# Kernel optimization log

Hardware: AMD Instinct MI355X
Metric: run time of the kernel (lower is better)

Reference implementation:

```python
import jax, jax.numpy as jnp
import numpy as np

HEADS = 8
DQK = 64
DV = 64
SPAN = 32
STRIDE = 1


def setup_inputs() -> dict:
    key = jax.random.key(0)
    ks = jax.random.split(key, 7)
    B, Lq, Lkv = 2, 4096, 4096
    dq = dk = dv = 512
    dout = 512
    w_scale = 0.02
    return {
        "q": jax.random.normal(ks[0], (B, Lq, dq), jnp.float32),
        "k": jax.random.normal(ks[1], (B, Lkv, dk), jnp.float32),
        "v": jax.random.normal(ks[2], (B, Lkv, dv), jnp.float32),
        "Wq": jax.random.normal(ks[3], (dq, HEADS * DQK), jnp.float32) * w_scale,
        "Wk": jax.random.normal(ks[4], (dk, HEADS * DQK), jnp.float32) * w_scale,
        "Wv": jax.random.normal(ks[5], (dv, HEADS * DV), jnp.float32) * w_scale,
        "Wo": jax.random.normal(ks[6], (HEADS * DV, dout), jnp.float32) * w_scale,
    }


def reference(q, k, v, Wq, Wk, Wv, Wo):
    B, Lq, _ = q.shape
    Lkv = k.shape[1]
    # projections -> [B, H, L, d]
    Q = (q @ Wq).reshape(B, Lq, HEADS, DQK).transpose(0, 2, 1, 3)
    K = (k @ Wk).reshape(B, Lkv, HEADS, DQK).transpose(0, 2, 1, 3)
    V = (v @ Wv).reshape(B, Lkv, HEADS, DV).transpose(0, 2, 1, 3)

    # sliding window indices: kvi[r, j] = r - (span-1) + stride*j  -> [span, Lq]
    r = jnp.arange(SPAN)
    j = jnp.arange(Lq)
    kvi = r[:, None] - (SPAN - 1) + STRIDE * j[None, :]
    valid = (kvi >= 0) & (kvi < Lkv)                      # [span, Lq]
    kvs = jnp.clip(kvi, 0, Lkv - 1)

    Kg = K[:, :, kvs, :]                                   # [B, H, span, Lq, dQK]
    scores = jnp.einsum("bhjd,bhrjd->bhrj", Q, Kg) / (DQK ** 0.5)
    scores = jnp.where(valid, scores, -jnp.inf)
    # faithful to original: softmax over dim=3 == length_q axis
    W = jax.nn.softmax(scores, axis=3)                     # [B, H, span, Lq]
    W = jnp.where(valid, W, 0.0)

    Vg = V[:, :, kvs, :]                                   # [B, H, span, Lq, dV]
    O = jnp.einsum("bhrj,bhrjd->bhjd", W, Vg)              # sum over span
    out = O.transpose(0, 2, 1, 3).reshape(B, Lq, HEADS * DV) @ Wo
    return out
```

## Files before the change

kernel.cpp:

```cpp
#include <hip/hip_runtime.h>
#include <hip/hip_bf16.h>

#define L_Q 4096
#define NB 2
#define DMODEL 512
#define NHEAD 8
#define DHEAD 64
#define SPAN_ 32

using short8 = __attribute__((ext_vector_type(8))) short;
using f32x4  = __attribute__((ext_vector_type(4))) float;

typedef __attribute__((address_space(1))) const void GV;
typedef __attribute__((address_space(3))) void LV;

__device__ __forceinline__ void gl2lds16(const void* g, void* l) {
    __builtin_amdgcn_global_load_lds((GV*)g, (LV*)l, 16, 0, 0);
}

__device__ __forceinline__ float bf2f(short u) {
    return __uint_as_float(((unsigned)(unsigned short)u) << 16);
}
__device__ __forceinline__ short f2bf(float f) {
    __hip_bfloat16 h = __float2bfloat16(f);
    return *reinterpret_cast<short*>(&h);
}
__device__ __forceinline__ unsigned packbf(float lo, float hi) {
    return (unsigned)(unsigned short)f2bf(lo) | ((unsigned)(unsigned short)f2bf(hi) << 16);
}

__global__ __launch_bounds__(256) void castT4_bf16(
    const float* __restrict__ Wq, const float* __restrict__ Wk,
    const float* __restrict__ Wv, const float* __restrict__ Wo,
    short* __restrict__ Wtq, short* __restrict__ Wtk,
    short* __restrict__ Wtv, short* __restrict__ Wto)
{
    const int z = blockIdx.z;
    const float* W = (z == 0) ? Wq : ((z == 1) ? Wk : ((z == 2) ? Wv : Wo));
    short* Wt = (z == 0) ? Wtq : ((z == 1) ? Wtk : ((z == 2) ? Wtv : Wto));
    __shared__ float t[32][33];
    const int tx = threadIdx.x, ty = threadIdx.y;
    const int bx = blockIdx.x, by = blockIdx.y;
#pragma unroll
    for (int i = 0; i < 4; ++i)
        t[ty + i * 8][tx] = W[(size_t)(by * 32 + ty + i * 8) * DMODEL + bx * 32 + tx];
    __syncthreads();
#pragma unroll
    for (int i = 0; i < 4; ++i)
        Wt[(size_t)(bx * 32 + ty + i * 8) * DMODEL + by * 32 + tx] = f2bf(t[tx][ty + i * 8]);
}

template<int OUTMODE, bool ACAST>
__device__ __forceinline__ void gemm128_body(
    const void* __restrict__ Avoid, const short* __restrict__ Bt, void* __restrict__ Cout,
    short* As, short* Bs)
{
    const int tid = threadIdx.x;
    const int m0 = blockIdx.y * 128;
    const int n0 = blockIdx.x * 128;
    const int w = tid >> 6, lane = tid & 63;
    const int wr = w & 1, wc = w >> 1;
    const int l15 = lane & 15, l4 = lane >> 4;

    f32x4 acc[4][4];
#pragma unroll
    for (int fm = 0; fm < 4; ++fm)
#pragma unroll
        for (int fn = 0; fn < 4; ++fn) acc[fm][fn] = (f32x4){0.f, 0.f, 0.f, 0.f};

    for (int k0 = 0; k0 < DMODEL; k0 += 64) {
        __syncthreads();
        if (ACAST) {
            const float* Af = (const float*)Avoid;
#pragma unroll
            for (int it = 0; it < 4; ++it) {
                int c = it * 256 + tid;
                int row = c >> 3, slot = c & 7;
                const float* src = Af + (size_t)(m0 + row) * DMODEL + k0 + slot * 8;
                float4 a = *(const float4*)src;
                float4 b = *(const float4*)(src + 4);
                short8 o;
                o[0] = f2bf(a.x); o[1] = f2bf(a.y); o[2] = f2bf(a.z); o[3] = f2bf(a.w);
                o[4] = f2bf(b.x); o[5] = f2bf(b.y); o[6] = f2bf(b.z); o[7] = f2bf(b.w);
                *(short8*)&As[(row * 8 + (slot ^ (row & 7))) * 8] = o;
            }
        } else {
            const short* Ab = (const short*)Avoid;
#pragma unroll
            for (int it = 0; it < 4; ++it) {
                int c = it * 256 + tid;
                int row = c >> 3, slot = c & 7;
                gl2lds16(Ab + (size_t)(m0 + row) * DMODEL + k0 + ((slot ^ (row & 7)) << 3), &As[c * 8]);
            }
        }
#pragma unroll
        for (int it = 0; it < 4; ++it) {
            int c = it * 256 + tid;
            int row = c >> 3, slot = c & 7;
            gl2lds16(Bt + (size_t)(n0 + row) * DMODEL + k0 + ((slot ^ (row & 7)) << 3), &Bs[c * 8]);
        }
        __syncthreads();
#pragma unroll
        for (int ks = 0; ks < 2; ++ks) {
            const int koff = ks * 4 + l4;
            short8 a[4], b[4];
#pragma unroll
            for (int fm = 0; fm < 4; ++fm) {
                int row = wr * 64 + fm * 16 + l15;
                a[fm] = *(const short8*)&As[(row * 8 + (koff ^ (row & 7))) * 8];
            }
#pragma unroll
            for (int fn = 0; fn < 4; ++fn) {
                int row = wc * 64 + fn * 16 + l15;
                b[fn] = *(const short8*)&Bs[(row * 8 + (koff ^ (row & 7))) * 8];
            }
#pragma unroll
            for (int fm = 0; fm < 4; ++fm)
#pragma unroll
                for (int fn = 0; fn < 4; ++fn)
                    acc[fm][fn] = __builtin_amdgcn_mfma_f32_16x16x32_bf16(
                        a[fm], b[fn], acc[fm][fn], 0, 0, 0);
        }
    }
#pragma unroll
    for (int fm = 0; fm < 4; ++fm)
#pragma unroll
        for (int fn = 0; fn < 4; ++fn) {
            if (OUTMODE == 2) {
                short4 o4;
                o4.x = f2bf(acc[fm][fn][0]);
                o4.y = f2bf(acc[fm][fn][1]);
                o4.z = f2bf(acc[fm][fn][2]);
                o4.w = f2bf(acc[fm][fn][3]);
                int m = m0 + wr * 64 + fm * 16 + l4 * 4;
                int bb = m >> 12, g = m & (L_Q - 1);
                int n = n0 + wc * 64 + fn * 16 + l15;
                int hh = n >> 6, dd = n & 63;
                *(short4*)&((short*)Cout)[(((size_t)bb * NHEAD + hh) * DHEAD + dd) * L_Q + g] = o4;
            } else {
#pragma unroll
                for (int i = 0; i < 4; ++i) {
                    size_t row = (size_t)(m0 + wr * 64 + fm * 16 + l4 * 4 + i);
                    int col = n0 + wc * 64 + fn * 16 + l15;
                    if (OUTMODE == 1) ((short*)Cout)[row * DMODEL + col] = f2bf(acc[fm][fn][i]);
                    else              ((float*)Cout)[row * DMODEL + col] = acc[fm][fn][i];
                }
            }
        }
}

__global__ __launch_bounds__(256) void gemm_qkv(
    const float* __restrict__ q, const float* __restrict__ k, const float* __restrict__ v,
    const short* __restrict__ Wtq, const short* __restrict__ Wtk, const short* __restrict__ Wtv,
    short* __restrict__ Qp, short* __restrict__ Kp, short* __restrict__ Vt)
{
    __shared__ short As[128 * 64];
    __shared__ short Bs[128 * 64];
    const int z = blockIdx.z;
    const float* A  = (z == 0) ? q   : ((z == 1) ? k   : v);
    const short* Bt = (z == 0) ? Wtq : ((z == 1) ? Wtk : Wtv);
    if (z == 2) gemm128_body<2, true>(A, Bt, Vt, As, Bs);
    else        gemm128_body<1, true>(A, Bt, (z == 0) ? Qp : Kp, As, Bs);
}

__global__ __launch_bounds__(256) void gemm_fin(
    const short* __restrict__ Op, const short* __restrict__ Wto, float* __restrict__ out)
{
    __shared__ short As[128 * 64];
    __shared__ short Bs[128 * 64];
    gemm128_body<0, false>(Op, Wto, out, As, Bs);
}

__global__ __launch_bounds__(256) void attn_e(
    const short* __restrict__ Qp, const short* __restrict__ Kp,
    float* __restrict__ part)
{
    __shared__ short Ks[160 * 64];
    __shared__ short Qs[128 * 64];
    __shared__ float eb[128][36];
    __shared__ float red[8][32];
    const int tid = threadIdx.x;
    const int j0 = blockIdx.x * 128;
    const int h = blockIdx.y, b = blockIdx.z;
    const int bh = b * NHEAD + h;
    const int w = tid >> 6, lane = tid & 63;
    const int l15 = lane & 15, l4 = lane >> 4;

    {
        float4 z = make_float4(0.f, 0.f, 0.f, 0.f);
        float4* ebv = (float4*)&eb[0][0];
#pragma unroll
        for (int i = 0; i < 5; ++i) {
            int idx = i * 256 + tid;
            if (idx < 1152) ebv[idx] = z;
        }
    }
#pragma unroll
    for (int it = 0; it < 5; ++it) {
        int c = it * 256 + tid;
        int row = c >> 3, slot = c & 7;
        int g = j0 - 31 + row;
        g = (g < 0) ? 0 : ((g > L_Q - 1) ? L_Q - 1 : g);
        gl2lds16(Kp + ((size_t)b * L_Q + g) * DMODEL + h * DHEAD + ((slot ^ (row & 7)) << 3), &Ks[c * 8]);
    }
#pragma unroll
    for (int it = 0; it < 4; ++it) {
        int c = it * 256 + tid;
        int row = c >> 3, slot = c & 7;
        gl2lds16(Qp + ((size_t)b * L_Q + j0 + row) * DMODEL + h * DHEAD + ((slot ^ (row & 7)) << 3), &Qs[c * 8]);
    }
    __syncthreads();

    f32x4 acc[2][4];
#pragma unroll
    for (int tm = 0; tm < 2; ++tm)
#pragma unroll
        for (int tn = 0; tn < 4; ++tn) acc[tm][tn] = (f32x4){0.f, 0.f, 0.f, 0.f};
#pragma unroll
    for (int kk = 0; kk < 2; ++kk) {
        const int koff = kk * 4 + l4;
        short8 af[2], bf[4];
#pragma unroll
        for (int tm = 0; tm < 2; ++tm) {
            int row = w * 32 + tm * 16 + l15;
            af[tm] = *(const short8*)&Qs[(row * 8 + (koff ^ (row & 7))) * 8];
        }
#pragma unroll
        for (int tn = 0; tn < 4; ++tn) {
            int row = w * 32 + tn * 16 + l15;
            bf[tn] = *(const short8*)&Ks[(row * 8 + (koff ^ (row & 7))) * 8];
        }
#pragma unroll
        for (int tm = 0; tm < 2; ++tm)
#pragma unroll
            for (int tn = 0; tn < 4; ++tn)
                acc[tm][tn] = __builtin_amdgcn_mfma_f32_16x16x32_bf16(
                    af[tm], bf[tn], acc[tm][tn], 0, 0, 0);
    }

    const int gbase = j0 + w * 32 - 31;
#pragma unroll
    for (int tm = 0; tm < 2; ++tm)
#pragma unroll
        for (int tn = 0; tn < 4; ++tn)
#pragma unroll
            for (int i = 0; i < 4; ++i) {
                int q = tm * 16 + l4 * 4 + i;
                int rr = tn * 16 + l15;
                int r = rr - q;
                bool valid = (r >= 0) && (r < SPAN_) && (gbase + rr >= 0);
                if (valid) eb[w * 32 + q][r] = __expf(acc[tm][tn][i] * 0.125f);
            }
    __syncthreads();

    {
        int r = tid & 31, grp = tid >> 5;
        float s = 0.f;
#pragma unroll
        for (int qq = 0; qq < 16; ++qq) s += eb[grp * 16 + qq][r];
        red[grp][r] = s;
    }
    __syncthreads();
    if (tid < 32) {
        float s = 0.f;
#pragma unroll
        for (int g = 0; g < 8; ++g) s += red[g][tid];
        part[((size_t)bh * SPAN_ + tid) * 32 + blockIdx.x] = s;
    }
}

__global__ __launch_bounds__(256) void attn_o(
    const short* __restrict__ Qp, const short* __restrict__ Kp,
    const short* __restrict__ Vt, const float* __restrict__ part,
    short* __restrict__ Op)
{
    __shared__ short Ks[160 * 64];
    __shared__ short Qs[128 * 64];
    __shared__ short Vts[64 * 192];
    const int tid = threadIdx.x;
    const int j0 = blockIdx.x * 128;
    const int h = blockIdx.y, b = blockIdx.z;
    const int bh = b * NHEAD + h;
    const int w = tid >> 6, lane = tid & 63;
    const int l15 = lane & 15, l4 = lane >> 4;

#pragma unroll
    for (int it = 0; it < 5; ++it) {
        int c = it * 256 + tid;
        int row = c >> 3, slot = c & 7;
        int g = j0 - 32 + row;
        g = (g < 0) ? 0 : ((g > L_Q - 1) ? L_Q - 1 : g);
        gl2lds16(Kp + ((size_t)b * L_Q + g) * DMODEL + h * DHEAD + ((slot ^ (row & 7)) << 3), &Ks[c * 8]);
    }
#pragma unroll
    for (int it = 0; it < 4; ++it) {
        int c = it * 256 + tid;
        int row = c >> 3, slot = c & 7;
        gl2lds16(Qp + ((size_t)b * L_Q + j0 + row) * DMODEL + h * DHEAD + ((slot ^ (row & 7)) << 3), &Qs[c * 8]);
    }
#pragma unroll
    for (int it = 0; it < 6; ++it) {
        int c = it * 256 + tid;
        int d = c / 24, cs = c - d * 24;
        int gg = j0 - 32 + ((cs ^ (d & 7)) << 3);
        gg = (gg < 0) ? 0 : ((gg > L_Q - 8) ? L_Q - 8 : gg);
        gl2lds16(Vt + ((size_t)bh * DHEAD + d) * L_Q + gg, &Vts[c * 8]);
    }

    float iv;
    {
        const float4* pp = (const float4*)(part + ((size_t)bh * SPAN_ + (lane & 31)) * 32);
        float s = 0.f;
#pragma unroll
        for (int i = 0; i < 8; ++i) {
            float4 t = pp[i];
            s += t.x + t.y + t.z + t.w;
        }
        iv = 1.0f / s;
    }
    __syncthreads();

    f32x4 sa[4][2];
#pragma unroll
    for (int tk = 0; tk < 4; ++tk)
#pragma unroll
        for (int tq = 0; tq < 2; ++tq) sa[tk][tq] = (f32x4){0.f, 0.f, 0.f, 0.f};
#pragma unroll
    for (int kk = 0; kk < 2; ++kk) {
        const int koff = kk * 4 + l4;
        short8 af[4], qf[2];
#pragma unroll
        for (int tk = 0; tk < 4; ++tk) {
            int row = w * 32 + tk * 16 + l15;
            af[tk] = *(const short8*)&Ks[(row * 8 + (koff ^ (row & 7))) * 8];
        }
#pragma unroll
        for (int tq = 0; tq < 2; ++tq) {
            int row = w * 32 + tq * 16 + l15;
            qf[tq] = *(const short8*)&Qs[(row * 8 + (koff ^ (row & 7))) * 8];
        }
#pragma unroll
        for (int tk = 0; tk < 4; ++tk)
#pragma unroll
            for (int tq = 0; tq < 2; ++tq)
                sa[tk][tq] = __builtin_amdgcn_mfma_f32_16x16x32_bf16(
                    af[tk], qf[tq], sa[tk][tq], 0, 0, 0);
    }

    const int gbase = j0 + w * 32 - 32;
#pragma unroll
    for (int tk = 0; tk < 4; ++tk)
#pragma unroll
        for (int tq = 0; tq < 2; ++tq)
#pragma unroll
            for (int i = 0; i < 4; ++i) {
                int rrp = tk * 16 + l4 * 4 + i;
                int q = tq * 16 + l15;
                int r = rrp - q - 1;
                bool valid = (r >= 0) && (r < SPAN_) && (gbase + rrp >= 0);
                float e = __expf(sa[tk][tq][i] * 0.125f) * __shfl(iv, r & 31);
                sa[tk][tq][i] = valid ? e : 0.f;
            }

    unsigned pk[4][2][2];
#pragma unroll
    for (int tk = 0; tk < 4; ++tk)
#pragma unroll
        for (int tq = 0; tq < 2; ++tq) {
            pk[tk][tq][0] = packbf(sa[tk][tq][0], sa[tk][tq][1]);
            pk[tk][tq][1] = packbf(sa[tk][tq][2], sa[tk][tq][3]);
        }

    const int hi = l4 >> 1;
    const int lsA = ((l4 & 1) << 5) + l15;

    f32x4 oa[2][4];
#pragma unroll
    for (int tm = 0; tm < 2; ++tm)
#pragma unroll
        for (int dn = 0; dn < 4; ++dn) oa[tm][dn] = (f32x4){0.f, 0.f, 0.f, 0.f};
#pragma unroll
    for (int kk = 0; kk < 2; ++kk) {
        short8 pa[2];
#pragma unroll
        for (int tm = 0; tm < 2; ++tm) {
            unsigned lo00 = (unsigned)__shfl((int)pk[kk * 2 + 0][tm][0], lsA);
            unsigned hi00 = (unsigned)__shfl((int)pk[kk * 2 + 1][tm][0], lsA);
            unsigned lo01 = (unsigned)__shfl((int)pk[kk * 2 + 0][tm][1], lsA);
            unsigned hi01 = (unsigned)__shfl((int)pk[kk * 2 + 1][tm][1], lsA);
            unsigned lo10 = (unsigned)__shfl((int)pk[kk * 2 + 0][tm][0], lsA + 16);
            unsigned hi10 = (unsigned)__shfl((int)pk[kk * 2 + 1][tm][0], lsA + 16);
            unsigned lo11 = (unsigned)__shfl((int)pk[kk * 2 + 0][tm][1], lsA + 16);
            unsigned hi11 = (unsigned)__shfl((int)pk[kk * 2 + 1][tm][1], lsA + 16);
            uint4 wds;
            wds.x = hi ? hi00 : lo00;
            wds.y = hi ? hi01 : lo01;
            wds.z = hi ? hi10 : lo10;
            wds.w = hi ? hi11 : lo11;
            pa[tm] = *reinterpret_cast<short8*>(&wds);
        }
#pragma unroll
        for (int dn = 0; dn < 4; ++dn) {
            int row = dn * 16 + l15;
            int cs = w * 4 + kk * 4 + l4;
            short8 vb = *(const short8*)&Vts[row * 192 + ((cs ^ (row & 7)) << 3)];
#pragma unroll
            for (int tm = 0; tm < 2; ++tm)
                oa[tm][dn] = __builtin_amdgcn_mfma_f32_16x16x32_bf16(
                    pa[tm], vb, oa[tm][dn], 0, 0, 0);
        }
    }

#pragma unroll
    for (int tm = 0; tm < 2; ++tm)
#pragma unroll
        for (int dn = 0; dn < 4; ++dn)
#pragma unroll
            for (int i = 0; i < 4; ++i) {
                int q = w * 32 + tm * 16 + l4 * 4 + i;
                Op[((size_t)b * L_Q + j0 + q) * DMODEL + h * DHEAD + dn * 16 + l15] =
                    f2bf(oa[tm][dn][i]);
            }
}

extern "C" void kernel_launch(void* const* d_in, const int* in_sizes, int n_in,
                              void* d_out, int out_size, void* d_ws, size_t ws_size,
                              hipStream_t stream) {
    (void)in_sizes; (void)n_in; (void)out_size; (void)ws_size;
    const float* q  = (const float*)d_in[0];
    const float* k  = (const float*)d_in[1];
    const float* v  = (const float*)d_in[2];
    const float* Wq = (const float*)d_in[3];
    const float* Wk = (const float*)d_in[4];
    const float* Wv = (const float*)d_in[5];
    const float* Wo = (const float*)d_in[6];
    float* out = (float*)d_out;

    char* ws = (char*)d_ws;
    const size_t MiB = 1ull << 20;
    short* Wtq = (short*)(ws);
    short* Wtk = (short*)(ws + 512 * 1024);
    short* Wtv = (short*)(ws + 1 * MiB);
    short* Wto = (short*)(ws + 1 * MiB + 512 * 1024);
    short* Qp  = (short*)(ws + 2 * MiB);
    short* Kp  = (short*)(ws + 10 * MiB);
    short* Vtp = (short*)(ws + 18 * MiB);
    short* Op  = (short*)(ws + 26 * MiB);
    float* part = (float*)(ws + 34 * MiB);

    castT4_bf16<<<dim3(16, 16, 4), dim3(32, 8), 0, stream>>>(
        Wq, Wk, Wv, Wo, Wtq, Wtk, Wtv, Wto);

    gemm_qkv<<<dim3(4, 64, 3), 256, 0, stream>>>(q, k, v, Wtq, Wtk, Wtv, Qp, Kp, Vtp);

    dim3 ga(L_Q / 128, NHEAD, NB);
    attn_e<<<ga, 256, 0, stream>>>(Qp, Kp, part);
    attn_o<<<ga, 256, 0, stream>>>(Qp, Kp, Vtp, part, Op);

    gemm_fin<<<dim3(4, 64), 256, 0, stream>>>(Op, Wto, out);
}
```

Baseline: 77.31 us.

## Prefetch fp32 A tiles into registers and swizzle GEMM blocks across XCDs

The GEMM body now loads the next k-slice of the fp32 A operand into registers while MFMAs on the current slice run, so global load latency for the cast path overlaps compute. Block indices are also remapped so that consecutive hardware block IDs (round-robined over the 8 XCDs) place the tiles of one M-row group on the same XCD, improving L2 reuse of A and B. This costs 32 extra VGPRs for the prefetch buffer, which may reduce occupancy. The swizzle hardcodes a 4x64 tile grid.

```diff
diff --git a/kernel.cpp b/kernel.cpp
--- a/kernel.cpp
+++ b/kernel.cpp
@@ -50,35 +50,52 @@
         Wt[(size_t)(bx * 32 + ty + i * 8) * DMODEL + by * 32 + tx] = f2bf(t[tx][ty + i * 8]);
 }
 
+__device__ __forceinline__ void xcd_swizzle(int& m0, int& n0) {
+    int hw = blockIdx.x + (blockIdx.y << 2);
+    int xcd = hw & 7, slot = hw >> 3;
+    int mt = xcd * 8 + (slot >> 2);
+    int nt = slot & 3;
+    m0 = mt * 128;
+    n0 = nt * 128;
+}
+
 template<int OUTMODE, bool ACAST>
 __device__ __forceinline__ void gemm128_body(
     const void* __restrict__ Avoid, const short* __restrict__ Bt, void* __restrict__ Cout,
-    short* As, short* Bs)
+    short* As, short* Bs, int m0, int n0)
 {
     const int tid = threadIdx.x;
-    const int m0 = blockIdx.y * 128;
-    const int n0 = blockIdx.x * 128;
     const int w = tid >> 6, lane = tid & 63;
     const int wr = w & 1, wc = w >> 1;
     const int l15 = lane & 15, l4 = lane >> 4;
+    const float* Af = (const float*)Avoid;
 
     f32x4 acc[4][4];
 #pragma unroll
     for (int fm = 0; fm < 4; ++fm)
 #pragma unroll
         for (int fn = 0; fn < 4; ++fn) acc[fm][fn] = (f32x4){0.f, 0.f, 0.f, 0.f};
+
+    float4 pf[8];
+    if (ACAST) {
+#pragma unroll
+        for (int it = 0; it < 4; ++it) {
+            int c = it * 256 + tid;
+            int row = c >> 3, slot = c & 7;
+            const float* src = Af + (size_t)(m0 + row) * DMODEL + slot * 8;
+            pf[it * 2 + 0] = *(const float4*)src;
+            pf[it * 2 + 1] = *(const float4*)(src + 4);
+        }
+    }
 
     for (int k0 = 0; k0 < DMODEL; k0 += 64) {
         __syncthreads();
         if (ACAST) {
-            const float* Af = (const float*)Avoid;
 #pragma unroll
             for (int it = 0; it < 4; ++it) {
                 int c = it * 256 + tid;
                 int row = c >> 3, slot = c & 7;
-                const float* src = Af + (size_t)(m0 + row) * DMODEL + k0 + slot * 8;
-                float4 a = *(const float4*)src;
-                float4 b = *(const float4*)(src + 4);
+                float4 a = pf[it * 2 + 0], b = pf[it * 2 + 1];
                 short8 o;
                 o[0] = f2bf(a.x); o[1] = f2bf(a.y); o[2] = f2bf(a.z); o[3] = f2bf(a.w);
                 o[4] = f2bf(b.x); o[5] = f2bf(b.y); o[6] = f2bf(b.z); o[7] = f2bf(b.w);
@@ -100,6 +117,16 @@
             gl2lds16(Bt + (size_t)(n0 + row) * DMODEL + k0 + ((slot ^ (row & 7)) << 3), &Bs[c * 8]);
         }
         __syncthreads();
+        if (ACAST && k0 + 64 < DMODEL) {
+#pragma unroll
+            for (int it = 0; it < 4; ++it) {
+                int c = it * 256 + tid;
+                int row = c >> 3, slot = c & 7;
+                const float* src = Af + (size_t)(m0 + row) * DMODEL + (k0 + 64) + slot * 8;
+                pf[it * 2 + 0] = *(const float4*)src;
+                pf[it * 2 + 1] = *(const float4*)(src + 4);
+            }
+        }
 #pragma unroll
         for (int ks = 0; ks < 2; ++ks) {
             const int koff = ks * 4 + l4;
@@ -156,11 +183,13 @@
 {
     __shared__ short As[128 * 64];
     __shared__ short Bs[128 * 64];
+    int m0, n0;
+    xcd_swizzle(m0, n0);
     const int z = blockIdx.z;
     const float* A  = (z == 0) ? q   : ((z == 1) ? k   : v);
     const short* Bt = (z == 0) ? Wtq : ((z == 1) ? Wtk : Wtv);
-    if (z == 2) gemm128_body<2, true>(A, Bt, Vt, As, Bs);
-    else        gemm128_body<1, true>(A, Bt, (z == 0) ? Qp : Kp, As, Bs);
+    if (z == 2) gemm128_body<2, true>(A, Bt, Vt, As, Bs, m0, n0);
+    else        gemm128_body<1, true>(A, Bt, (z == 0) ? Qp : Kp, As, Bs, m0, n0);
 }
 
 __global__ __launch_bounds__(256) void gemm_fin(
@@ -168,7 +197,9 @@
 {
     __shared__ short As[128 * 64];
     __shared__ short Bs[128 * 64];
-    gemm128_body<0, false>(Op, Wto, out, As, Bs);
+    int m0, n0;
+    xcd_swizzle(m0, n0);
+    gemm128_body<0, false>(Op, Wto, out, As, Bs, m0, n0);
 }
 
 __global__ __launch_bounds__(256) void attn_e(
```

Measured after the change: 63.25 us (median of 2 runs). 18.2% less time.

## Load fp32 A tiles via direct-to-LDS and swizzle GEMM blocks across XCDs

Applied to the files above, without the earlier changes.

The QKV projection GEMM now streams fp32 activations straight into LDS with async global_load_lds and converts them to bf16 when it reads fragments, instead of loading into registers, converting, and storing to LDS. Both GEMMs also remap block indices so that consecutive M tiles sharing the same rows land on the same XCD, which is meant to improve L2 reuse. In exchange, the fp32 A tile doubles LDS use to 32KB and the conversion now runs redundantly inside the MFMA inner loop. The swizzle hardcodes a grid of 4 N tiles by 64 M tiles.

```diff
diff --git a/kernel.cpp b/kernel.cpp
--- a/kernel.cpp
+++ b/kernel.cpp
@@ -50,17 +50,26 @@
         Wt[(size_t)(bx * 32 + ty + i * 8) * DMODEL + by * 32 + tx] = f2bf(t[tx][ty + i * 8]);
 }
 
-template<int OUTMODE, bool ACAST>
+__device__ __forceinline__ void xcd_swizzle(int& m0, int& n0) {
+    int hw = blockIdx.x + (blockIdx.y << 2);
+    int xcd = hw & 7, slot = hw >> 3;
+    int mt = xcd * 8 + (slot >> 2);
+    int nt = slot & 3;
+    m0 = mt * 128;
+    n0 = nt * 128;
+}
+
+template<int OUTMODE, bool AF32>
 __device__ __forceinline__ void gemm128_body(
     const void* __restrict__ Avoid, const short* __restrict__ Bt, void* __restrict__ Cout,
-    short* As, short* Bs)
+    void* AsRaw, short* Bs, int m0, int n0)
 {
     const int tid = threadIdx.x;
-    const int m0 = blockIdx.y * 128;
-    const int n0 = blockIdx.x * 128;
     const int w = tid >> 6, lane = tid & 63;
     const int wr = w & 1, wc = w >> 1;
     const int l15 = lane & 15, l4 = lane >> 4;
+    float* Asf = (float*)AsRaw;
+    short* Asb = (short*)AsRaw;
 
     f32x4 acc[4][4];
 #pragma unroll
@@ -70,27 +79,23 @@
 
     for (int k0 = 0; k0 < DMODEL; k0 += 64) {
         __syncthreads();
-        if (ACAST) {
+        if (AF32) {
             const float* Af = (const float*)Avoid;
+#pragma unroll
+            for (int it = 0; it < 8; ++it) {
+                int c = it * 256 + tid;
+                int row = c >> 4, slot = c & 15;
+                gl2lds16(Af + (size_t)(m0 + row) * DMODEL + k0 + ((slot ^ (row & 15)) << 2),
+                         &Asf[c * 4]);
+            }
+        } else {
+            const short* Ab = (const short*)Avoid;
 #pragma unroll
             for (int it = 0; it < 4; ++it) {
                 int c = it * 256 + tid;
                 int row = c >> 3, slot = c & 7;
-                const float* src = Af + (size_t)(m0 + row) * DMODEL + k0 + slot * 8;
-                float4 a = *(const float4*)src;
-                float4 b = *(const float4*)(src + 4);
-                short8 o;
-                o[0] = f2bf(a.x); o[1] = f2bf(a.y); o[2] = f2bf(a.z); o[3] = f2bf(a.w);
-                o[4] = f2bf(b.x); o[5] = f2bf(b.y); o[6] = f2bf(b.z); o[7] = f2bf(b.w);
-                *(short8*)&As[(row * 8 + (slot ^ (row & 7))) * 8] = o;
-            }
-        } else {
-            const short* Ab = (const short*)Avoid;
-#pragma unroll
-            for (int it = 0; it < 4; ++it) {
-                int c = it * 256 + tid;
-                int row = c >> 3, slot = c & 7;
-                gl2lds16(Ab + (size_t)(m0 + row) * DMODEL + k0 + ((slot ^ (row & 7)) << 3), &As[c * 8]);
+                gl2lds16(Ab + (size_t)(m0 + row) * DMODEL + k0 + ((slot ^ (row & 7)) << 3),
+                         &Asb[c * 8]);
             }
         }
 #pragma unroll
@@ -107,7 +112,17 @@
 #pragma unroll
             for (int fm = 0; fm < 4; ++fm) {
                 int row = wr * 64 + fm * 16 + l15;
-                a[fm] = *(const short8*)&As[(row * 8 + (koff ^ (row & 7))) * 8];
+                if (AF32) {
+                    int rx = row & 15;
+                    float4 f0 = *(const float4*)&Asf[row * 64 + (((koff * 2)     ^ rx) << 2)];
+                    float4 f1 = *(const float4*)&Asf[row * 64 + (((koff * 2 + 1) ^ rx) << 2)];
+                    short8 o;
+                    o[0] = f2bf(f0.x); o[1] = f2bf(f0.y); o[2] = f2bf(f0.z); o[3] = f2bf(f0.w);
+                    o[4] = f2bf(f1.x); o[5] = f2bf(f1.y); o[6] = f2bf(f1.z); o[7] = f2bf(f1.w);
+                    a[fm] = o;
+                } else {
+                    a[fm] = *(const short8*)&Asb[(row * 8 + (koff ^ (row & 7))) * 8];
+                }
             }
 #pragma unroll
             for (int fn = 0; fn < 4; ++fn) {
@@ -154,13 +169,15 @@
     const short* __restrict__ Wtq, const short* __restrict__ Wtk, const short* __restrict__ Wtv,
     short* __restrict__ Qp, short* __restrict__ Kp, short* __restrict__ Vt)
 {
-    __shared__ short As[128 * 64];
+    __shared__ float Asf[128 * 64];
     __shared__ short Bs[128 * 64];
+    int m0, n0;
+    xcd_swizzle(m0, n0);
     const int z = blockIdx.z;
     const float* A  = (z == 0) ? q   : ((z == 1) ? k   : v);
     const short* Bt = (z == 0) ? Wtq : ((z == 1) ? Wtk : Wtv);
-    if (z == 2) gemm128_body<2, true>(A, Bt, Vt, As, Bs);
-    else        gemm128_body<1, true>(A, Bt, (z == 0) ? Qp : Kp, As, Bs);
+    if (z == 2) gemm128_body<2, true>(A, Bt, Vt, Asf, Bs, m0, n0);
+    else        gemm128_body<1, true>(A, Bt, (z == 0) ? Qp : Kp, Asf, Bs, m0, n0);
 }
 
 __global__ __launch_bounds__(256) void gemm_fin(
@@ -168,7 +185,9 @@
 {
     __shared__ short As[128 * 64];
     __shared__ short Bs[128 * 64];
-    gemm128_body<0, false>(Op, Wto, out, As, Bs);
+    int m0, n0;
+    xcd_swizzle(m0, n0);
+    gemm128_body<0, false>(Op, Wto, out, As, Bs, m0, n0);
 }
 
 __global__ __launch_bounds__(256) void attn_e(
```

Measured after the change: 64.18 us. 1.2x faster.
